# Kernel tuning notes

Measured on AMD Instinct MI355X. Metric: run time of the kernel, lower is better.

Reference implementation:

```python
import jax, jax.numpy as jnp
import numpy as np

N = 100000   # nodes
F = 128      # feature dim (== numEdges ctor arg)
H = 64       # hidden_dim
E = 1600000  # edges (avg degree 16)


def setup_inputs() -> dict:
    key = jax.random.key(0)
    ks = jax.random.split(key, 8)
    x = jax.random.normal(ks[0], (N, F), dtype=jnp.float32)
    edge_index = jax.random.randint(ks[1], (2, E), 0, N)
    sF = 1.0 / np.sqrt(F)
    sH = 1.0 / np.sqrt(H)
    conv_W = jax.random.normal(ks[2], (F, F), dtype=jnp.float32) * sF  # GCNConv linear weight
    conv_b = jnp.zeros((F,), dtype=jnp.float32)
    w1 = jax.random.normal(ks[3], (H, F), dtype=jnp.float32) * sF
    b1 = jnp.zeros((H,), dtype=jnp.float32)
    w2 = jax.random.normal(ks[4], (H, H), dtype=jnp.float32) * sH
    b2 = jnp.zeros((H,), dtype=jnp.float32)
    w3 = jax.random.normal(ks[5], (1, H), dtype=jnp.float32) * sH
    b3 = jnp.zeros((1,), dtype=jnp.float32)
    return dict(x=x, edge_index=edge_index, conv_W=conv_W, conv_b=conv_b,
                w1=w1, b1=b1, w2=w2, b2=b2, w3=w3, b3=b3)


def reference(x, edge_index, conv_W, conv_b, w1, b1, w2, b2, w3, b3):
    n = x.shape[0]
    # --- GCNConv: D^{-1/2}(A+I)D^{-1/2} X W + b ---
    xw = x @ conv_W.T                                   # [N, F]
    loops = jnp.arange(n)
    src = jnp.concatenate([edge_index[0], loops])       # add self-loops
    dst = jnp.concatenate([edge_index[1], loops])
    deg = jax.ops.segment_sum(jnp.ones(src.shape[0], xw.dtype), dst, num_segments=n)
    dinv = jnp.where(deg > 0, jax.lax.rsqrt(deg), 0.0)
    norm = dinv[src] * dinv[dst]                        # [E+N]
    h = jax.ops.segment_sum(xw[src] * norm[:, None], dst, num_segments=n) + conv_b  # [N, F]
    # --- MedianAggregation (index=None -> single segment, 'lower' interpolation) ---
    med = jnp.sort(h, axis=0)[(n - 1) // 2][None, :]    # [1, F]
    # --- tanh MLP ---
    a = jnp.tanh(med @ w1.T + b1)
    a = jnp.tanh(a @ w2.T + b2)
    return a @ w3.T + b3                                # [1, 1]
```

## Files before the change

kernel.cpp:

```cpp
#include <hip/hip_runtime.h>
#include <math.h>


#define CAP    24576
#define MPT    24
#define CCAP   96
#define CSTR   97
#define DSTR   32
#define OVCAP  4096
#define SPCAP  2048
#define BCAP   4608
#define NBKMAX 400
#define CH     4096

typedef __attribute__((ext_vector_type(8))) short short8;
typedef __attribute__((ext_vector_type(4))) float f32x4;
typedef __attribute__((ext_vector_type(8))) _Float16 half8;
typedef __attribute__((ext_vector_type(2))) _Float16 half2v;

__device__ __forceinline__ unsigned ordKey(float x) {
    unsigned u = __float_as_uint(x);
    return (u & 0x80000000u) ? ~u : (u | 0x80000000u);
}
__device__ __forceinline__ unsigned short f2bf(float f) {
    unsigned u = __float_as_uint(f);
    return (unsigned short)((u + 0x7FFFu + ((u >> 16) & 1u)) >> 16);
}

__global__ void k_init(int* __restrict__ cursor, int* __restrict__ below,
                       int* __restrict__ candCnt, int* __restrict__ ovCnt,
                       const float* __restrict__ W, short* __restrict__ Whi,
                       short* __restrict__ Wlo, int nbk) {
    if (blockIdx.x == 1) {
        for (int idx = threadIdx.x; idx < 16384; idx += 256) {
            int j = idx & 7, lane = (idx >> 3) & 63;
            int t = (idx >> 9) & 7, s = idx >> 12;
            int row = t * 16 + (lane & 15);
            int k = s * 32 + (lane >> 4) * 8 + j;
            float w = W[row * 128 + k];
            unsigned short hb = f2bf(w);
            float hf = __uint_as_float((unsigned)hb << 16);
            Whi[idx] = (short)hb;
            Wlo[idx] = (short)f2bf(w - hf);
        }
        return;
    }
    int t = threadIdx.x;
    for (int i = t; i < nbk; i += 256) cursor[i] = 0;
    if (t < 128) { below[t] = 0; candCnt[t] = 0; }
    if (t == 0) { ovCnt[0] = 0; ovCnt[1] = 0; ovCnt[2] = 0; }
}

__global__ __launch_bounds__(256) void k_gemm(
        const float* __restrict__ x, const short* __restrict__ Whi,
        const short* __restrict__ Wlo, _Float16* __restrict__ xw, int n) {
    __shared__ float trn[4 * 16 * 132];
    const int t = threadIdx.x;
    const int lane = t & 63, wv = t >> 6;
    const int quad = lane >> 4, m = lane & 15;
    const int rowBase = blockIdx.x * 64 + wv * 16;
    const int r = rowBase + m;
    const int rl = r < n ? r : (n - 1);
    f32x4 acc[8];
    #pragma unroll
    for (int q = 0; q < 8; q++) acc[q] = (f32x4){0.f, 0.f, 0.f, 0.f};
    #pragma unroll
    for (int s = 0; s < 4; s++) {
        const float* xp = x + (size_t)rl * 128 + s * 32 + quad * 8;
        float4 p0 = *(const float4*)xp;
        float4 p1 = *(const float4*)(xp + 4);
        float f[8] = {p0.x, p0.y, p0.z, p0.w, p1.x, p1.y, p1.z, p1.w};
        short8 ah, al;
        #pragma unroll
        for (int j = 0; j < 8; j++) {
            unsigned short hb = f2bf(f[j]);
            float hf = __uint_as_float((unsigned)hb << 16);
            ah[j] = (short)hb;
            al[j] = (short)f2bf(f[j] - hf);
        }
        #pragma unroll
        for (int q = 0; q < 8; q++) {
            short8 bh = *(const short8*)(Whi + (((s * 8 + q) * 64 + lane) << 3));
            short8 bl = *(const short8*)(Wlo + (((s * 8 + q) * 64 + lane) << 3));
            acc[q] = __builtin_amdgcn_mfma_f32_16x16x32_bf16(ah, bh, acc[q], 0, 0, 0);
            acc[q] = __builtin_amdgcn_mfma_f32_16x16x32_bf16(al, bh, acc[q], 0, 0, 0);
            acc[q] = __builtin_amdgcn_mfma_f32_16x16x32_bf16(ah, bl, acc[q], 0, 0, 0);
        }
    }
    float* tw = trn + wv * (16 * 132);
    #pragma unroll
    for (int q = 0; q < 8; q++)
        #pragma unroll
        for (int e = 0; e < 4; e++)
            tw[(quad * 4 + e) * 132 + q * 16 + m] = acc[q][e];
    #pragma unroll
    for (int i = 0; i < 4; i++) {
        int row = i * 4 + (lane >> 4);
        int c8 = lane & 15;
        const float* tp = tw + row * 132 + c8 * 8;
        float4 p0 = *(const float4*)tp;
        float4 p1 = *(const float4*)(tp + 4);
        half8 o;
        o[0] = (_Float16)p0.x; o[1] = (_Float16)p0.y;
        o[2] = (_Float16)p0.z; o[3] = (_Float16)p0.w;
        o[4] = (_Float16)p1.x; o[5] = (_Float16)p1.y;
        o[6] = (_Float16)p1.z; o[7] = (_Float16)p1.w;
        int grow = rowBase + row;
        if (grow < n) *(half8*)(xw + (size_t)grow * 128 + c8 * 8) = o;
    }
}

__global__ __launch_bounds__(256) void k_bin(
        const int* __restrict__ src, const int* __restrict__ dst, int E,
        int* __restrict__ cursor, int2* __restrict__ binned,
        int* __restrict__ ovCnt, int2* __restrict__ ovBuf, int nbk) {
    __shared__ char smem[39168];
    const int t = threadIdx.x;
    int2* stage = (int2*)smem;
    int* hist  = (int*)(smem + 32768);
    int* gbase = hist + NBKMAX;
    int* hist2 = gbase + NBKMAX;
    int* sbase = hist2 + NBKMAX;
    const int e0 = (int)blockIdx.x * CH;
    const int len = min(CH, E - e0);
    for (int i = t; i < nbk; i += 256) { hist[i] = 0; hist2[i] = 0; }
    __syncthreads();
    for (int k = t; k < len; k += 256) {
        int s = src[e0 + k], d = dst[e0 + k];
        stage[k] = make_int2(s, d);
        atomicAdd(&hist[d >> 8], 1);
    }
    __syncthreads();
    for (int i = t; i < nbk; i += 256) {
        int c = hist[i];
        if (c) {
            int g = atomicAdd(&cursor[i], c);
            if (g + c <= BCAP) gbase[i] = g;
            else {
                gbase[i] = -1;
                sbase[i] = atomicAdd(ovCnt, c);
            }
        }
    }
    __syncthreads();
    for (int k = t; k < len; k += 256) {
        int2 e = stage[k];
        int b = e.y >> 8;
        int p = atomicAdd(&hist2[b], 1);
        int g = gbase[b];
        if (g >= 0) binned[(size_t)b * BCAP + g + p] = e;
        else {
            int o = sbase[b] + p;
            if (o < OVCAP) ovBuf[o] = make_int2(e.y, e.x);
        }
    }
}

__global__ __launch_bounds__(512) void k_build(int2* __restrict__ binned,
                                               const int* __restrict__ cursor,
                                               float* __restrict__ dinv,
                                               unsigned char* __restrict__ deg8,
                                               int* __restrict__ ovCnt,
                                               int2* __restrict__ ovBuf,
                                               int* __restrict__ spillNodes, int n) {
    __shared__ int ladj[256 * DSTR];
    __shared__ int lcnt[256];
    const int b = blockIdx.x, t = threadIdx.x;
    const int cnt = min(cursor[b], BCAP);
    const size_t e0 = (size_t)b * BCAP;
    if (t < 256) lcnt[t] = 0;
    __syncthreads();
    for (int k = t; k < cnt; k += 512) {
        int2 e = binned[e0 + k];
        int li = e.y & 255;
        int pos = atomicAdd(&lcnt[li], 1);
        if (pos < DSTR) ladj[li * DSTR + pos] = e.x;
        else {
            int o = atomicAdd(ovCnt, 1);
            if (o < OVCAP) ovBuf[o] = make_int2(e.y, e.x);
        }
    }
    __syncthreads();
    int4* adjOut = (int4*)((int*)binned + e0 * 2);
    const int4* lsrc4 = (const int4*)ladj;
    for (int i = t; i < 2048; i += 512) adjOut[i] = lsrc4[i];
    if (t < 256) {
        int node = b * 256 + t;
        if (node < n) {
            int deg = lcnt[t];
            dinv[node] = (float)(1.0 / sqrt((double)(deg + 1)));
            deg8[node] = (unsigned char)(deg < 255 ? deg : 255);
            if (deg > DSTR) {
                int p = atomicAdd(ovCnt + 1, 1);
                if (p < SPCAP) spillNodes[p] = node;
            }
        }
    }
}

__global__ __launch_bounds__(256) void k_aggH(const _Float16* __restrict__ xw,
                                              const unsigned char* __restrict__ deg8,
                                              const int* __restrict__ adjAll,
                                              const float* __restrict__ dinv,
                                              const float* __restrict__ conv_b,
                                              _Float16* __restrict__ h,
                                              int n0, int n1) {
    const int d = n0 + blockIdx.x * 4 + (threadIdx.x >> 6);
    if (d >= n1) return;
    const int lane = threadIdx.x & 63;
    const int l32 = lane & 31;
    int degT = deg8[d];
    const int degB = degT < DSTR ? degT : DSTR;
    const float dd = dinv[d];
    const int* adjRow = adjAll + (size_t)(d >> 8) * (BCAP * 2) + (d & 255) * DSTR;
    int aj = adjRow[l32];
    bool ev = (lane < 32) && (l32 < degB);
    int ajs = ev ? aj : 0;
    float dv = ev ? dinv[ajs] : 0.f;
    const half2v* xwv = (const half2v*)xw;
    half2v a = xwv[(size_t)d * 64 + lane];
    float ax = dd * dd * (float)a.x, ay = dd * dd * (float)a.y;
    int j = 0;
    for (; j + 8 <= degB; j += 8) {
        int s[8];
        float w[8];
        #pragma unroll
        for (int q = 0; q < 8; q++) {
            s[q] = __shfl(ajs, j + q, 64);
            w[q] = dd * __shfl(dv, j + q, 64);
        }
        #pragma unroll
        for (int q = 0; q < 8; q++) {
            half2v v = xwv[(size_t)s[q] * 64 + lane];
            ax += w[q] * (float)v.x;
            ay += w[q] * (float)v.y;
        }
    }
    if (j < degB) {
        int s[8];
        float w[8];
        #pragma unroll
        for (int q = 0; q < 8; q++) {
            int idx = j + q;
            bool ok = idx < degB;
            int lsrc = ok ? idx : 0;
            int sv = __shfl(ajs, lsrc, 64);
            float wv = dd * __shfl(dv, lsrc, 64);
            s[q] = ok ? sv : 0;
            w[q] = ok ? wv : 0.f;
        }
        #pragma unroll
        for (int q = 0; q < 8; q++) {
            half2v v = xwv[(size_t)s[q] * 64 + lane];
            ax += w[q] * (float)v.x;
            ay += w[q] * (float)v.y;
        }
    }
    float2 cb = ((const float2*)conv_b)[lane];
    half2v o;
    o.x = (_Float16)(ax + cb.x);
    o.y = (_Float16)(ay + cb.y);
    ((half2v*)h)[(size_t)d * 64 + lane] = o;
}

__global__ __launch_bounds__(256) void k_sampleSpill(
        _Float16* h, int n,
        unsigned* __restrict__ Lkey, unsigned* __restrict__ Ukey,
        const _Float16* __restrict__ xw, const int* __restrict__ spillNodes,
        const int* __restrict__ adjAll, const float* __restrict__ dinv,
        const float* __restrict__ conv_b, const int2* __restrict__ ovBuf,
        const int* __restrict__ ovCnt) {
    const int t = threadIdx.x;
    if (blockIdx.x >= 128) {
        int m = ovCnt[0];  if (m > OVCAP) m = OVCAP;
        int sp = ovCnt[1]; if (sp > SPCAP) sp = SPCAP;
        if (t >= 128) return;
        for (int i = (int)blockIdx.x - 128; i < sp; i += 16) {
            const int d = spillNodes[i];
            const float dd = dinv[d];
            float acc = dd * dd * (float)xw[(size_t)d * 128 + t];
            const int* adjRow = adjAll + (size_t)(d >> 8) * (BCAP * 2) + (d & 255) * DSTR;
            for (int j = 0; j < DSTR; j++) {
                int a = adjRow[j];
                acc += dd * dinv[a] * (float)xw[(size_t)a * 128 + t];
            }
            for (int k = 0; k < m; k++) {
                int2 e = ovBuf[k];
                if (e.x == d)
                    acc += dd * dinv[e.y] * (float)xw[(size_t)e.y * 128 + t];
            }
            h[(size_t)d * 128 + t] = (_Float16)(acc + conv_b[t]);
        }
        return;
    }
    __shared__ int hist[2048];
    __shared__ int wsum[4];
    const int c = blockIdx.x;
    for (int i = t; i < 2048; i += 256) hist[i] = 0;
    __syncthreads();
    const int ns = (n + 31) >> 5;
    for (int i = t; i < ns; i += 256) {
        float v = (float)h[(size_t)(i << 5) * 128 + c];
        atomicAdd(&hist[ordKey(v) >> 21], 1);
    }
    __syncthreads();
    int ps = 0;
    #pragma unroll
    for (int b = 0; b < 8; b++) ps += hist[t * 8 + b];
    const int lane = t & 63, wv = t >> 6;
    int sc = ps;
    #pragma unroll
    for (int off = 1; off < 64; off <<= 1) {
        int y = __shfl_up(sc, off, 64);
        if (lane >= off) sc += y;
    }
    if (lane == 63) wsum[wv] = sc;
    __syncthreads();
    int wbase = 0;
    for (int ww = 0; ww < wv; ww++) wbase += wsum[ww];
    const int excl = wbase + sc - ps;
    const int sMid = (ns - 1) >> 1;
    const int delta = (int)(4.0f * sqrtf((float)ns)) + 1;
    int sLo = sMid - delta; if (sLo < 0) sLo = 0;
    int sHi = sMid + delta; if (sHi > ns - 1) sHi = ns - 1;
    if (sLo >= excl && sLo < excl + ps) {
        int rem = sLo - excl, b = t * 8;
        for (;; b++) { int cc = hist[b]; if (rem < cc) break; rem -= cc; }
        Lkey[c] = (unsigned)b << 21;
    }
    if (sHi >= excl && sHi < excl + ps) {
        int rem = sHi - excl, b = t * 8;
        for (;; b++) { int cc = hist[b]; if (rem < cc) break; rem -= cc; }
        Ukey[c] = (((unsigned)(b + 1)) << 21) - 1u;
    }
}

__global__ __launch_bounds__(256) void k_classify(const _Float16* __restrict__ h,
                                                  int total8,
                                                  const unsigned* __restrict__ Lkey,
                                                  const unsigned* __restrict__ Ukey,
                                                  int* __restrict__ below,
                                                  int* __restrict__ candCnt,
                                                  _Float16* __restrict__ cand) {
    __shared__ _Float16 buf[128 * CSTR];
    __shared__ int cN[128], cB[128];
    const int t = threadIdx.x;
    for (int i = t; i < 128; i += 256) { cN[i] = 0; cB[i] = 0; }
    __syncthreads();
    const int stride = gridDim.x * blockDim.x;
    const int i0 = blockIdx.x * blockDim.x + t;
    const int jb = (i0 << 3) & 127;
    unsigned L[8], U[8];
    #pragma unroll
    for (int k = 0; k < 8; k++) { L[k] = Lkey[jb + k]; U[k] = Ukey[jb + k]; }
    int b[8] = {0, 0, 0, 0, 0, 0, 0, 0};
    const half8* hv = (const half8*)h;
    for (int i = i0; i < total8; i += stride) {
        half8 v = hv[i];
        #pragma unroll
        for (int k = 0; k < 8; k++) {
            float f = (float)v[k];
            unsigned u = ordKey(f);
            if (u < L[k]) b[k]++;
            else if (u <= U[k]) {
                int p = atomicAdd(&cN[jb + k], 1);
                if (p < CCAP) buf[(jb + k) * CSTR + p] = v[k];
                else {
                    int g = atomicAdd(&candCnt[jb + k], 1);
                    if (g < CAP) cand[(size_t)(jb + k) * CAP + g] = v[k];
                }
            }
        }
    }
    #pragma unroll
    for (int k = 0; k < 8; k++)
        if (b[k]) atomicAdd(&cB[jb + k], b[k]);
    __syncthreads();
    if (t < 128) {
        if (cB[t]) atomicAdd(&below[t], cB[t]);
        int nn = cN[t] < CCAP ? cN[t] : CCAP;
        if (nn) {
            int base = atomicAdd(&candCnt[t], nn);
            for (int k2 = 0; k2 < nn && base + k2 < CAP; k2++)
                cand[(size_t)t * CAP + base + k2] = buf[t * CSTR + k2];
        }
    }
}

__global__ __launch_bounds__(1024) void k_finalMlp(
        const _Float16* __restrict__ cand, const int* __restrict__ candCnt,
        const int* __restrict__ below, int n, float* __restrict__ med,
        int* __restrict__ doneCnt,
        const float* __restrict__ w1, const float* __restrict__ b1,
        const float* __restrict__ w2, const float* __restrict__ b2,
        const float* __restrict__ w3, const float* __restrict__ b3,
        float* __restrict__ out) {
    __shared__ int wsum[16];
    __shared__ int lastFlag;
    const int c = blockIdx.x, t = threadIdx.x;
    const int lane = t & 63, wv = t >> 6;
    int cnt = candCnt[c]; if (cnt > CAP) cnt = CAP;
    const unsigned short* cp = (const unsigned short*)cand + (size_t)c * CAP;
    int r = (n - 1) / 2 - below[c];
    if (r < 0) r = 0;
    if (r >= cnt) r = cnt - 1;
    unsigned short myk[MPT];
    #pragma unroll
    for (int mi = 0; mi < MPT; mi++) {
        int i = t + mi * 1024;
        unsigned ub = (i < cnt) ? (unsigned)cp[i] : 0u;
        unsigned k = (ub & 0x8000u) ? (~ub & 0xFFFFu) : (ub | 0x8000u);
        myk[mi] = (i < cnt) ? (unsigned short)k : (unsigned short)0xFFFFu;
    }
    unsigned cur = 0;
    for (int bit = 15; bit >= 0; bit--) {
        const unsigned pivot = cur | (1u << bit);
        int lc = 0;
        #pragma unroll
        for (int mi = 0; mi < MPT; mi++) lc += ((unsigned)myk[mi] < pivot) ? 1 : 0;
        #pragma unroll
        for (int off = 32; off > 0; off >>= 1) lc += __shfl_down(lc, off, 64);
        if (lane == 0) wsum[wv] = lc;
        __syncthreads();
        int tot = 0;
        #pragma unroll
        for (int ww = 0; ww < 16; ww++) tot += wsum[ww];
        if (tot <= r) cur = pivot;
        __syncthreads();
    }
    if (t == 0) {
        unsigned short bits = (cur & 0x8000u) ? (unsigned short)(cur & 0x7FFFu)
                                              : (unsigned short)(~cur & 0xFFFFu);
        _Float16 hv;
        *(unsigned short*)&hv = bits;
        med[c] = (float)hv;
        __threadfence();
        int old = atomicAdd(doneCnt, 1);
        lastFlag = (old == 127);
    }
    __syncthreads();
    if (!lastFlag) return;
    __threadfence();
    __shared__ float m[128], a1[64], a2[64];
    if (t < 128) m[t] = med[t];
    __syncthreads();
    if (t < 64) {
        float acc = b1[t];
        for (int f = 0; f < 128; f++) acc += m[f] * w1[t * 128 + f];
        a1[t] = tanhf(acc);
    }
    __syncthreads();
    if (t < 64) {
        float acc = b2[t];
        for (int f = 0; f < 64; f++) acc += a1[f] * w2[t * 64 + f];
        a2[t] = tanhf(acc);
    }
    __syncthreads();
    if (t == 0) {
        float acc = b3[0];
        for (int f = 0; f < 64; f++) acc += a2[f] * w3[f];
        out[0] = acc;
    }
}

extern "C" void kernel_launch(void* const* d_in, const int* in_sizes, int n_in,
                              void* d_out, int out_size, void* d_ws, size_t ws_size,
                              hipStream_t stream) {
    const float* x      = (const float*)d_in[0];
    const int*   ei     = (const int*)d_in[1];
    const float* conv_W = (const float*)d_in[2];
    const float* conv_b = (const float*)d_in[3];
    const float* w1 = (const float*)d_in[4];
    const float* b1 = (const float*)d_in[5];
    const float* w2 = (const float*)d_in[6];
    const float* b2 = (const float*)d_in[7];
    const float* w3 = (const float*)d_in[8];
    const float* b3 = (const float*)d_in[9];

    const int N = in_sizes[0] / 128;
    const int E = in_sizes[1] / 2;
    const int* src = ei;
    const int* dst = ei + E;
    const int NBK = (N + 255) / 256;

    char* p = (char*)d_ws;
    auto alloc = [&](size_t bytes) -> char* {
        char* q = p;
        p += (bytes + 255) & ~(size_t)255;
        return q;
    };
    _Float16* xw  = (_Float16*)alloc((size_t)N * 128 * 2);
    _Float16* h   = (_Float16*)alloc((size_t)N * 128 * 2);
    int2*  binned = (int2*)alloc((size_t)NBK * BCAP * 8);
    _Float16* cand = (_Float16*)alloc((size_t)128 * CAP * 2);
    float* dinv   = (float*)alloc((size_t)N * 4);
    unsigned char* deg8 = (unsigned char*)alloc((size_t)N);
    int*   cursor = (int*)alloc((size_t)NBK * 4);
    short* Whi    = (short*)alloc(16384 * 2);
    short* Wlo    = (short*)alloc(16384 * 2);
    int2*  ovBuf  = (int2*)alloc((size_t)OVCAP * 8);
    int*   ovCnt  = (int*)alloc(256);
    int*   spillNodes = (int*)alloc((size_t)SPCAP * 4);
    unsigned* Lkey = (unsigned*)alloc(128 * 4);
    unsigned* Ukey = (unsigned*)alloc(128 * 4);
    int*   below   = (int*)alloc(128 * 4);
    int*   candCnt = (int*)alloc(128 * 4);
    float* med     = (float*)alloc(128 * 4);

    const int GB   = (N + 63) / 64;
    const int BINB = (E + CH - 1) / CH;
    const int NH   = ((N / 2) + 3) & ~3;

    k_init<<<2, 256, 0, stream>>>(cursor, below, candCnt, ovCnt, conv_W, Whi, Wlo, NBK);
    k_gemm<<<GB, 256, 0, stream>>>(x, Whi, Wlo, xw, N);
    k_bin<<<BINB, 256, 0, stream>>>(src, dst, E, cursor, binned, ovCnt, ovBuf, NBK);
    k_build<<<NBK, 512, 0, stream>>>(binned, cursor, dinv, deg8, ovCnt, ovBuf,
                                     spillNodes, N);
    k_aggH<<<(NH + 3) / 4, 256, 0, stream>>>(xw, deg8, (const int*)binned, dinv,
                                             conv_b, h, 0, NH);
    k_aggH<<<(N - NH + 3) / 4, 256, 0, stream>>>(xw, deg8, (const int*)binned, dinv,
                                                 conv_b, h, NH, N);
    k_sampleSpill<<<144, 256, 0, stream>>>(h, N, Lkey, Ukey, xw, spillNodes,
                                           (const int*)binned, dinv, conv_b,
                                           ovBuf, ovCnt);
    k_classify<<<512, 256, 0, stream>>>(h, N * 16, Lkey, Ukey, below, candCnt, cand);
    k_finalMlp<<<128, 1024, 0, stream>>>(cand, candCnt, below, N, med, ovCnt + 2,
                                         w1, b1, w2, b2, w3, b3, (float*)d_out);
}
```

Before: 299.9 us.

## Fuse GEMM and edge binning into one launch, shard candidate counters

Merges the GEMM and edge-binning kernels into a single launch, with block index deciding the role, so both independent stages run concurrently and one launch is removed. The two half-range aggregation launches become one launch. k_build goes from 512 to 1024 threads per block. The global candidate and below counters in classify are split into 8 regions keyed by block id, which reduces atomic contention, and finalMlp sums across regions. Each region holds at most 3072 candidates per column, which could overflow on skewed data where one shared 24576 buffer would not.

```diff
diff --git a/kernel.cpp b/kernel.cpp
--- a/kernel.cpp
+++ b/kernel.cpp
@@ -3,6 +3,8 @@
 
 
 #define CAP    24576
+#define NREG   8
+#define RCAP   3072
 #define MPT    24
 #define CCAP   96
 #define CSTR   97
@@ -27,8 +29,8 @@
     return (unsigned short)((u + 0x7FFFu + ((u >> 16) & 1u)) >> 16);
 }
 
-__global__ void k_init(int* __restrict__ cursor, int* __restrict__ below,
-                       int* __restrict__ candCnt, int* __restrict__ ovCnt,
+__global__ void k_init(int* __restrict__ cursor, int* __restrict__ below8,
+                       int* __restrict__ candCnt8, int* __restrict__ ovCnt,
                        const float* __restrict__ W, short* __restrict__ Whi,
                        short* __restrict__ Wlo, int nbk) {
     if (blockIdx.x == 1) {
@@ -47,122 +49,121 @@
     }
     int t = threadIdx.x;
     for (int i = t; i < nbk; i += 256) cursor[i] = 0;
-    if (t < 128) { below[t] = 0; candCnt[t] = 0; }
+    for (int i = t; i < NREG * 128; i += 256) { below8[i] = 0; candCnt8[i] = 0; }
     if (t == 0) { ovCnt[0] = 0; ovCnt[1] = 0; ovCnt[2] = 0; }
 }
 
-__global__ __launch_bounds__(256) void k_gemm(
+__global__ __launch_bounds__(256) void k_binGemm(
         const float* __restrict__ x, const short* __restrict__ Whi,
-        const short* __restrict__ Wlo, _Float16* __restrict__ xw, int n) {
-    __shared__ float trn[4 * 16 * 132];
-    const int t = threadIdx.x;
-    const int lane = t & 63, wv = t >> 6;
-    const int quad = lane >> 4, m = lane & 15;
-    const int rowBase = blockIdx.x * 64 + wv * 16;
-    const int r = rowBase + m;
-    const int rl = r < n ? r : (n - 1);
-    f32x4 acc[8];
-    #pragma unroll
-    for (int q = 0; q < 8; q++) acc[q] = (f32x4){0.f, 0.f, 0.f, 0.f};
-    #pragma unroll
-    for (int s = 0; s < 4; s++) {
-        const float* xp = x + (size_t)rl * 128 + s * 32 + quad * 8;
-        float4 p0 = *(const float4*)xp;
-        float4 p1 = *(const float4*)(xp + 4);
-        float f[8] = {p0.x, p0.y, p0.z, p0.w, p1.x, p1.y, p1.z, p1.w};
-        short8 ah, al;
-        #pragma unroll
-        for (int j = 0; j < 8; j++) {
-            unsigned short hb = f2bf(f[j]);
-            float hf = __uint_as_float((unsigned)hb << 16);
-            ah[j] = (short)hb;
-            al[j] = (short)f2bf(f[j] - hf);
-        }
-        #pragma unroll
-        for (int q = 0; q < 8; q++) {
-            short8 bh = *(const short8*)(Whi + (((s * 8 + q) * 64 + lane) << 3));
-            short8 bl = *(const short8*)(Wlo + (((s * 8 + q) * 64 + lane) << 3));
-            acc[q] = __builtin_amdgcn_mfma_f32_16x16x32_bf16(ah, bh, acc[q], 0, 0, 0);
-            acc[q] = __builtin_amdgcn_mfma_f32_16x16x32_bf16(al, bh, acc[q], 0, 0, 0);
-            acc[q] = __builtin_amdgcn_mfma_f32_16x16x32_bf16(ah, bl, acc[q], 0, 0, 0);
-        }
-    }
-    float* tw = trn + wv * (16 * 132);
-    #pragma unroll
-    for (int q = 0; q < 8; q++)
-        #pragma unroll
-        for (int e = 0; e < 4; e++)
-            tw[(quad * 4 + e) * 132 + q * 16 + m] = acc[q][e];
-    #pragma unroll
-    for (int i = 0; i < 4; i++) {
-        int row = i * 4 + (lane >> 4);
-        int c8 = lane & 15;
-        const float* tp = tw + row * 132 + c8 * 8;
-        float4 p0 = *(const float4*)tp;
-        float4 p1 = *(const float4*)(tp + 4);
-        half8 o;
-        o[0] = (_Float16)p0.x; o[1] = (_Float16)p0.y;
-        o[2] = (_Float16)p0.z; o[3] = (_Float16)p0.w;
-        o[4] = (_Float16)p1.x; o[5] = (_Float16)p1.y;
-        o[6] = (_Float16)p1.z; o[7] = (_Float16)p1.w;
-        int grow = rowBase + row;
-        if (grow < n) *(half8*)(xw + (size_t)grow * 128 + c8 * 8) = o;
-    }
-}
-
-__global__ __launch_bounds__(256) void k_bin(
+        const short* __restrict__ Wlo, _Float16* __restrict__ xw, int n, int GB,
         const int* __restrict__ src, const int* __restrict__ dst, int E,
         int* __restrict__ cursor, int2* __restrict__ binned,
         int* __restrict__ ovCnt, int2* __restrict__ ovBuf, int nbk) {
     __shared__ char smem[39168];
     const int t = threadIdx.x;
-    int2* stage = (int2*)smem;
-    int* hist  = (int*)(smem + 32768);
-    int* gbase = hist + NBKMAX;
-    int* hist2 = gbase + NBKMAX;
-    int* sbase = hist2 + NBKMAX;
-    const int e0 = (int)blockIdx.x * CH;
-    const int len = min(CH, E - e0);
-    for (int i = t; i < nbk; i += 256) { hist[i] = 0; hist2[i] = 0; }
-    __syncthreads();
-    for (int k = t; k < len; k += 256) {
-        int s = src[e0 + k], d = dst[e0 + k];
-        stage[k] = make_int2(s, d);
-        atomicAdd(&hist[d >> 8], 1);
-    }
-    __syncthreads();
-    for (int i = t; i < nbk; i += 256) {
-        int c = hist[i];
-        if (c) {
-            int g = atomicAdd(&cursor[i], c);
-            if (g + c <= BCAP) gbase[i] = g;
+    if ((int)blockIdx.x < GB) {
+        float* trn = (float*)smem;
+        const int lane = t & 63, wv = t >> 6;
+        const int quad = lane >> 4, m = lane & 15;
+        const int rowBase = blockIdx.x * 64 + wv * 16;
+        const int r = rowBase + m;
+        const int rl = r < n ? r : (n - 1);
+        f32x4 acc[8];
+        #pragma unroll
+        for (int q = 0; q < 8; q++) acc[q] = (f32x4){0.f, 0.f, 0.f, 0.f};
+        #pragma unroll
+        for (int s = 0; s < 4; s++) {
+            const float* xp = x + (size_t)rl * 128 + s * 32 + quad * 8;
+            float4 p0 = *(const float4*)xp;
+            float4 p1 = *(const float4*)(xp + 4);
+            float f[8] = {p0.x, p0.y, p0.z, p0.w, p1.x, p1.y, p1.z, p1.w};
+            short8 ah, al;
+            #pragma unroll
+            for (int j = 0; j < 8; j++) {
+                unsigned short hb = f2bf(f[j]);
+                float hf = __uint_as_float((unsigned)hb << 16);
+                ah[j] = (short)hb;
+                al[j] = (short)f2bf(f[j] - hf);
+            }
+            #pragma unroll
+            for (int q = 0; q < 8; q++) {
+                short8 bh = *(const short8*)(Whi + (((s * 8 + q) * 64 + lane) << 3));
+                short8 bl = *(const short8*)(Wlo + (((s * 8 + q) * 64 + lane) << 3));
+                acc[q] = __builtin_amdgcn_mfma_f32_16x16x32_bf16(ah, bh, acc[q], 0, 0, 0);
+                acc[q] = __builtin_amdgcn_mfma_f32_16x16x32_bf16(al, bh, acc[q], 0, 0, 0);
+                acc[q] = __builtin_amdgcn_mfma_f32_16x16x32_bf16(ah, bl, acc[q], 0, 0, 0);
+            }
+        }
+        float* tw = trn + wv * (16 * 132);
+        #pragma unroll
+        for (int q = 0; q < 8; q++)
+            #pragma unroll
+            for (int e = 0; e < 4; e++)
+                tw[(quad * 4 + e) * 132 + q * 16 + m] = acc[q][e];
+        #pragma unroll
+        for (int i = 0; i < 4; i++) {
+            int row = i * 4 + (lane >> 4);
+            int c8 = lane & 15;
+            const float* tp = tw + row * 132 + c8 * 8;
+            float4 p0 = *(const float4*)tp;
+            float4 p1 = *(const float4*)(tp + 4);
+            half8 o;
+            o[0] = (_Float16)p0.x; o[1] = (_Float16)p0.y;
+            o[2] = (_Float16)p0.z; o[3] = (_Float16)p0.w;
+            o[4] = (_Float16)p1.x; o[5] = (_Float16)p1.y;
+            o[6] = (_Float16)p1.z; o[7] = (_Float16)p1.w;
+            int grow = rowBase + row;
+            if (grow < n) *(half8*)(xw + (size_t)grow * 128 + c8 * 8) = o;
+        }
+    } else {
+        int2* stage = (int2*)smem;
+        int* hist  = (int*)(smem + 32768);
+        int* gbase = hist + NBKMAX;
+        int* hist2 = gbase + NBKMAX;
+        int* sbase = hist2 + NBKMAX;
+        const int e0 = ((int)blockIdx.x - GB) * CH;
+        const int len = min(CH, E - e0);
+        for (int i = t; i < nbk; i += 256) { hist[i] = 0; hist2[i] = 0; }
+        __syncthreads();
+        for (int k = t; k < len; k += 256) {
+            int s = src[e0 + k], d = dst[e0 + k];
+            stage[k] = make_int2(s, d);
+            atomicAdd(&hist[d >> 8], 1);
+        }
+        __syncthreads();
+        for (int i = t; i < nbk; i += 256) {
+            int c = hist[i];
+            if (c) {
+                int g = atomicAdd(&cursor[i], c);
+                if (g + c <= BCAP) gbase[i] = g;
+                else {
+                    gbase[i] = -1;
+                    sbase[i] = atomicAdd(ovCnt, c);
+                }
+            }
+        }
+        __syncthreads();
+        for (int k = t; k < len; k += 256) {
+            int2 e = stage[k];
+            int b = e.y >> 8;
+            int p = atomicAdd(&hist2[b], 1);
+            int g = gbase[b];
+            if (g >= 0) binned[(size_t)b * BCAP + g + p] = e;
             else {
-                gbase[i] = -1;
-                sbase[i] = atomicAdd(ovCnt, c);
-            }
-        }
-    }
-    __syncthreads();
-    for (int k = t; k < len; k += 256) {
-        int2 e = stage[k];
-        int b = e.y >> 8;
-        int p = atomicAdd(&hist2[b], 1);
-        int g = gbase[b];
-        if (g >= 0) binned[(size_t)b * BCAP + g + p] = e;
-        else {
-            int o = sbase[b] + p;
-            if (o < OVCAP) ovBuf[o] = make_int2(e.y, e.x);
-        }
-    }
-}
-
-__global__ __launch_bounds__(512) void k_build(int2* __restrict__ binned,
-                                               const int* __restrict__ cursor,
-                                               float* __restrict__ dinv,
-                                               unsigned char* __restrict__ deg8,
-                                               int* __restrict__ ovCnt,
-                                               int2* __restrict__ ovBuf,
-                                               int* __restrict__ spillNodes, int n) {
+                int o = sbase[b] + p;
+                if (o < OVCAP) ovBuf[o] = make_int2(e.y, e.x);
+            }
+        }
+    }
+}
+
+__global__ __launch_bounds__(1024) void k_build(int2* __restrict__ binned,
+                                                const int* __restrict__ cursor,
+                                                float* __restrict__ dinv,
+                                                unsigned char* __restrict__ deg8,
+                                                int* __restrict__ ovCnt,
+                                                int2* __restrict__ ovBuf,
+                                                int* __restrict__ spillNodes, int n) {
     __shared__ int ladj[256 * DSTR];
     __shared__ int lcnt[256];
     const int b = blockIdx.x, t = threadIdx.x;
@@ -170,7 +171,7 @@
     const size_t e0 = (size_t)b * BCAP;
     if (t < 256) lcnt[t] = 0;
     __syncthreads();
-    for (int k = t; k < cnt; k += 512) {
+    for (int k = t; k < cnt; k += 1024) {
         int2 e = binned[e0 + k];
         int li = e.y & 255;
         int pos = atomicAdd(&lcnt[li], 1);
@@ -183,7 +184,7 @@
     __syncthreads();
     int4* adjOut = (int4*)((int*)binned + e0 * 2);
     const int4* lsrc4 = (const int4*)ladj;
-    for (int i = t; i < 2048; i += 512) adjOut[i] = lsrc4[i];
+    for (int i = t; i < 2048; i += 1024) adjOut[i] = lsrc4[i];
     if (t < 256) {
         int node = b * 256 + t;
         if (node < n) {
@@ -203,10 +204,9 @@
                                               const int* __restrict__ adjAll,
                                               const float* __restrict__ dinv,
                                               const float* __restrict__ conv_b,
-                                              _Float16* __restrict__ h,
-                                              int n0, int n1) {
-    const int d = n0 + blockIdx.x * 4 + (threadIdx.x >> 6);
-    if (d >= n1) return;
+                                              _Float16* __restrict__ h, int n) {
+    const int d = blockIdx.x * 4 + (threadIdx.x >> 6);
+    if (d >= n) return;
     const int lane = threadIdx.x & 63;
     const int l32 = lane & 31;
     int degT = deg8[d];
@@ -339,12 +339,13 @@
                                                   int total8,
                                                   const unsigned* __restrict__ Lkey,
                                                   const unsigned* __restrict__ Ukey,
-                                                  int* __restrict__ below,
-                                                  int* __restrict__ candCnt,
+                                                  int* __restrict__ below8,
+                                                  int* __restrict__ candCnt8,
                                                   _Float16* __restrict__ cand) {
     __shared__ _Float16 buf[128 * CSTR];
     __shared__ int cN[128], cB[128];
     const int t = threadIdx.x;
+    const int rid = (int)blockIdx.x & (NREG - 1);
     for (int i = t; i < 128; i += 256) { cN[i] = 0; cB[i] = 0; }
     __syncthreads();
     const int stride = gridDim.x * blockDim.x;
@@ -366,8 +367,9 @@
                 int p = atomicAdd(&cN[jb + k], 1);
                 if (p < CCAP) buf[(jb + k) * CSTR + p] = v[k];
                 else {
-                    int g = atomicAdd(&candCnt[jb + k], 1);
-                    if (g < CAP) cand[(size_t)(jb + k) * CAP + g] = v[k];
+                    int g = atomicAdd(&candCnt8[rid * 128 + jb + k], 1);
+                    if (g < RCAP)
+                        cand[(size_t)(jb + k) * CAP + rid * RCAP + g] = v[k];
                 }
             }
         }
@@ -377,19 +379,19 @@
         if (b[k]) atomicAdd(&cB[jb + k], b[k]);
     __syncthreads();
     if (t < 128) {
-        if (cB[t]) atomicAdd(&below[t], cB[t]);
+        if (cB[t]) atomicAdd(&below8[rid * 128 + t], cB[t]);
         int nn = cN[t] < CCAP ? cN[t] : CCAP;
         if (nn) {
-            int base = atomicAdd(&candCnt[t], nn);
-            for (int k2 = 0; k2 < nn && base + k2 < CAP; k2++)
-                cand[(size_t)t * CAP + base + k2] = buf[t * CSTR + k2];
+            int base = atomicAdd(&candCnt8[rid * 128 + t], nn);
+            for (int k2 = 0; k2 < nn && base + k2 < RCAP; k2++)
+                cand[(size_t)t * CAP + rid * RCAP + base + k2] = buf[t * CSTR + k2];
         }
     }
 }
 
 __global__ __launch_bounds__(1024) void k_finalMlp(
-        const _Float16* __restrict__ cand, const int* __restrict__ candCnt,
-        const int* __restrict__ below, int n, float* __restrict__ med,
+        const _Float16* __restrict__ cand, const int* __restrict__ candCnt8,
+        const int* __restrict__ below8, int n, float* __restrict__ med,
         int* __restrict__ doneCnt,
         const float* __restrict__ w1, const float* __restrict__ b1,
         const float* __restrict__ w2, const float* __restrict__ b2,
@@ -399,19 +401,29 @@
     __shared__ int lastFlag;
     const int c = blockIdx.x, t = threadIdx.x;
     const int lane = t & 63, wv = t >> 6;
-    int cnt = candCnt[c]; if (cnt > CAP) cnt = CAP;
-    const unsigned short* cp = (const unsigned short*)cand + (size_t)c * CAP;
-    int r = (n - 1) / 2 - below[c];
+    int below_tot = 0;
+    #pragma unroll
+    for (int rr = 0; rr < NREG; rr++) below_tot += below8[rr * 128 + c];
+    int cnt = 0;
+    unsigned short myk[MPT];
+    const unsigned short* cbase = (const unsigned short*)cand + (size_t)c * CAP;
+    #pragma unroll
+    for (int rr = 0; rr < NREG; rr++) {
+        int cr = candCnt8[rr * 128 + c]; if (cr > RCAP) cr = RCAP;
+        cnt += cr;
+        const unsigned short* rp = cbase + rr * RCAP;
+        #pragma unroll
+        for (int k = 0; k < RCAP / 1024; k++) {
+            int i = t + k * 1024;
+            unsigned ub = (i < cr) ? (unsigned)rp[i] : 0u;
+            unsigned kk = (ub & 0x8000u) ? (~ub & 0xFFFFu) : (ub | 0x8000u);
+            myk[rr * (RCAP / 1024) + k] =
+                (i < cr) ? (unsigned short)kk : (unsigned short)0xFFFFu;
+        }
+    }
+    int r = (n - 1) / 2 - below_tot;
     if (r < 0) r = 0;
     if (r >= cnt) r = cnt - 1;
-    unsigned short myk[MPT];
-    #pragma unroll
-    for (int mi = 0; mi < MPT; mi++) {
-        int i = t + mi * 1024;
-        unsigned ub = (i < cnt) ? (unsigned)cp[i] : 0u;
-        unsigned k = (ub & 0x8000u) ? (~ub & 0xFFFFu) : (ub | 0x8000u);
-        myk[mi] = (i < cnt) ? (unsigned short)k : (unsigned short)0xFFFFu;
-    }
     unsigned cur = 0;
     for (int bit = 15; bit >= 0; bit--) {
         const unsigned pivot = cur | (1u << bit);
@@ -503,27 +515,28 @@
     int*   spillNodes = (int*)alloc((size_t)SPCAP * 4);
     unsigned* Lkey = (unsigned*)alloc(128 * 4);
     unsigned* Ukey = (unsigned*)alloc(128 * 4);
-    int*   below   = (int*)alloc(128 * 4);
-    int*   candCnt = (int*)alloc(128 * 4);
+    int*   below8   = (int*)alloc((size_t)NREG * 128 * 4);
+    int*   candCnt8 = (int*)alloc((size_t)NREG * 128 * 4);
     float* med     = (float*)alloc(128 * 4);
 
     const int GB   = (N + 63) / 64;
     const int BINB = (E + CH - 1) / CH;
-    const int NH   = ((N / 2) + 3) & ~3;
-
-    k_init<<<2, 256, 0, stream>>>(cursor, below, candCnt, ovCnt, conv_W, Whi, Wlo, NBK);
-    k_gemm<<<GB, 256, 0, stream>>>(x, Whi, Wlo, xw, N);
-    k_bin<<<BINB, 256, 0, stream>>>(src, dst, E, cursor, binned, ovCnt, ovBuf, NBK);
-    k_build<<<NBK, 512, 0, stream>>>(binned, cursor, dinv, deg8, ovCnt, ovBuf,
-                                     spillNodes, N);
-    k_aggH<<<(NH + 3) / 4, 256, 0, stream>>>(xw, deg8, (const int*)binned, dinv,
-                                             conv_b, h, 0, NH);
-    k_aggH<<<(N - NH + 3) / 4, 256, 0, stream>>>(xw, deg8, (const int*)binned, dinv,
-                                                 conv_b, h, NH, N);
+
+    k_init<<<2, 256, 0, stream>>>(cursor, below8, candCnt8, ovCnt, conv_W,
+                                  Whi, Wlo, NBK);
+    k_binGemm<<<GB + BINB, 256, 0, stream>>>(x, Whi, Wlo, xw, N, GB,
+                                             src, dst, E, cursor, binned,
+                                             ovCnt, ovBuf, NBK);
+    k_build<<<NBK, 1024, 0, stream>>>(binned, cursor, dinv, deg8, ovCnt, ovBuf,
+                                      spillNodes, N);
+    k_aggH<<<(N + 3) / 4, 256, 0, stream>>>(xw, deg8, (const int*)binned, dinv,
+                                            conv_b, h, N);
     k_sampleSpill<<<144, 256, 0, stream>>>(h, N, Lkey, Ukey, xw, spillNodes,
                                            (const int*)binned, dinv, conv_b,
                                            ovBuf, ovCnt);
-    k_classify<<<512, 256, 0, stream>>>(h, N * 16, Lkey, Ukey, below, candCnt, cand);
-    k_finalMlp<<<128, 1024, 0, stream>>>(cand, candCnt, below, N, med, ovCnt + 2,
-                                         w1, b1, w2, b2, w3, b3, (float*)d_out);
-}
+    k_classify<<<512, 256, 0, stream>>>(h, N * 16, Lkey, Ukey, below8, candCnt8,
+                                        cand);
+    k_finalMlp<<<128, 1024, 0, stream>>>(cand, candCnt8, below8, N, med,
+                                         ovCnt + 2, w1, b1, w2, b2, w3, b3,
+                                         (float*)d_out);
+}
```

Measured after the change: 276.0 us. -8.0%, faster.
